# Kernel tuning notes

Hardware: AMD Instinct MI355X
Metric: run time of the kernel (lower is better)

## Reference

```python
import jax, jax.numpy as jnp
import numpy as np

B, N, QD = 2, 2048, 1024
HEADS, DIM_HEAD = 16, 64
INNER = HEADS * DIM_HEAD  # 1024
SCALE = DIM_HEAD ** -0.5


def setup_inputs() -> dict:
    key = jax.random.key(0)
    ks = jax.random.split(key, 8)
    x = jax.random.normal(ks[0], (B, N, QD), dtype=jnp.float32)
    bias = jax.random.normal(ks[1], (B, N, N), dtype=jnp.float32)
    mask = jax.random.randint(ks[2], (B, N), 0, 2) > 0
    # parameters (nn.Linear stores weight [out, in]; we keep [in, out] and matmul x @ W)
    Wq = jax.random.normal(ks[3], (QD, INNER), dtype=jnp.float32) * (QD ** -0.5)
    Wkv = jax.random.normal(ks[4], (QD, 2 * INNER), dtype=jnp.float32) * (QD ** -0.5)
    Wo = jax.random.normal(ks[5], (INNER, QD), dtype=jnp.float32) * (INNER ** -0.5)
    bo = jax.random.normal(ks[6], (QD,), dtype=jnp.float32) * 0.01
    return {"x": x, "bias": bias, "mask": mask, "Wq": Wq, "Wkv": Wkv, "Wo": Wo, "bo": bo}


def reference(x, bias, mask, Wq, Wkv, Wo, bo):
    b, n, _ = x.shape
    q = x @ Wq                      # [b, n, inner]
    kv = x @ Wkv                    # [b, n, 2*inner] (context defaults to x)
    k, v = jnp.split(kv, 2, axis=-1)
    # split heads: [b, h, n, d]
    split = lambda t: t.reshape(b, n, HEADS, DIM_HEAD).transpose(0, 2, 1, 3)
    q, k, v = split(q), split(k), split(v)
    sim = jnp.einsum('bhid,bhjd->bhij', q, k) * SCALE   # [b, h, n, n]
    sim = sim + bias[:, None, :, :]                      # additive bias broadcast over heads
    max_neg = -jnp.finfo(sim.dtype).max
    sim = jnp.where(mask[:, None, None, :], sim, max_neg)  # per-key mask
    attn = jax.nn.softmax(sim, axis=-1)
    out = jnp.einsum('bhij,bhjd->bhid', attn, v)         # [b, h, n, d]
    out = out.transpose(0, 2, 1, 3).reshape(b, n, INNER)  # merge heads
    return out @ Wo + bo
```

## Files before the change

kernel.cpp:

```cpp
#include <hip/hip_runtime.h>
#include <hip/hip_bf16.h>
#include <stdint.h>

#define B_     2
#define N_     2048
#define QD_    1024
#define H_     16
#define DH_    64
#define INNER_ 1024
#define SCALE_ 0.125f

typedef unsigned short u16;
typedef __attribute__((ext_vector_type(8))) short bf16x8;
typedef __attribute__((ext_vector_type(4))) float f32x4;
typedef __attribute__((ext_vector_type(4))) unsigned short u16x4;
typedef __attribute__((ext_vector_type(8))) unsigned short u16x8;

#define GLD16(gp, lp) __builtin_amdgcn_global_load_lds( \
    (const __attribute__((address_space(1))) unsigned int*)(gp), \
    (__attribute__((address_space(3))) unsigned int*)(lp), 16, 0, 0)

__device__ inline u16 f2bf(float f) {
    union { float f; uint32_t u; } c; c.f = f;
    uint32_t r = c.u + 0x7FFFu + ((c.u >> 16) & 1u);
    return (u16)(r >> 16);
}
__device__ inline float bf2f(u16 s) {
    union { uint32_t u; float f; } c; c.u = ((uint32_t)s) << 16;
    return c.f;
}
__device__ inline void split2(float v, u16 &h, u16 &l) {
    u16 hs = f2bf(v);
    h = hs;
    l = f2bf(v - bf2f(hs));
}
__device__ inline unsigned pk2(float a, float b) {
    float2 f; f.x = a; f.y = b;
    union { __hip_bfloat162 v; unsigned u; } c;
    c.v = __float22bfloat162_rn(f);
    return c.u;
}
__device__ inline float f4get(const float4& v, int r) {
    return r == 0 ? v.x : r == 1 ? v.y : r == 2 ? v.z : v.w;
}

__global__ __launch_bounds__(256) void prep_kernel(
    const float* __restrict__ x, u16* __restrict__ xh, u16* __restrict__ xl,
    const float* __restrict__ Wq, const float* __restrict__ Wkv, const float* __restrict__ Wo,
    u16* __restrict__ wTh, u16* __restrict__ wTl,
    u16* __restrict__ woTh, u16* __restrict__ woTl)
{
    __shared__ float t[32][33];
    const int blk = blockIdx.x, tid = threadIdx.x;
    if (blk < 4096) {
        int idx = blk * 256 + tid;
        float4 v = ((const float4*)x)[idx];
        u16x4 hv, lv; u16 h, l;
        split2(v.x, h, l); hv.x = h; lv.x = l;
        split2(v.y, h, l); hv.y = h; lv.y = l;
        split2(v.z, h, l); hv.z = h; lv.z = l;
        split2(v.w, h, l); hv.w = h; lv.w = l;
        ((u16x4*)xh)[idx] = hv;
        ((u16x4*)xl)[idx] = lv;
        return;
    }
    int local = blk - 4096;
    const float* src; u16 *dhi, *dlo; int C, bx, by;
    if (local < 1024)      { src = Wq;  dhi = wTh;                dlo = wTl;                C = 1024; by = local >> 5; bx = local & 31; }
    else if (local < 3072) { int l2 = local - 1024; src = Wkv; dhi = wTh + 1024 * 1024; dlo = wTl + 1024 * 1024; C = 2048; by = l2 >> 6; bx = l2 & 63; }
    else                   { int l2 = local - 3072; src = Wo;  dhi = woTh;               dlo = woTl;               C = 1024; by = l2 >> 5; bx = l2 & 31; }
    const int x0 = bx * 32, y0 = by * 32;
    const int tx = tid & 31, ty = tid >> 5;
    for (int yy = ty; yy < 32; yy += 8)
        t[yy][tx] = src[(size_t)(y0 + yy) * C + x0 + tx];
    __syncthreads();
    for (int i = ty; i < 32; i += 8) {
        float v = t[tx][i];
        u16 h, l; split2(v, h, l);
        size_t o = (size_t)(x0 + i) * 1024 + y0 + tx;
        dhi[o] = h; dlo[o] = l;
    }
}

__device__ inline void bias_read(int T, int bkoff, int bl16,
                                 const float* __restrict__ bias,
                                 const int* __restrict__ mask,
                                 float4 bR[4], int4& bM)
{
    int bb2 = T >> 10, rest = T & 1023;
    int k0b = (rest & 31) * 64, q0 = (rest >> 5) * 64;
    int kk = k0b + bkoff;
    bM = *(const int4*)&mask[bb2 * N_ + kk];
#pragma unroll
    for (int m = 0; m < 4; m++)
        bR[m] = *(const float4*)&bias[((size_t)bb2 * N_ + q0 + m * 16 + bl16) * N_ + kk];
}
__device__ inline void bias_store(int T, int bwvr, int blane, int bhf,
                                  const float4 bR[4], const int4& bM,
                                  u16* __restrict__ bsw)
{
    int bb2 = T >> 10, rest = T & 1023;
    int k0b = (rest & 31) * 64, q0 = (rest >> 5) * 64;
    int wv = ((k0b >> 5) & 3) + bwvr;
    const u16 NEG = f2bf(-1e30f);
    const int mok[4] = { bM.x, bM.y, bM.z, bM.w };
    u16x8 o0, o1;
#pragma unroll
    for (int i = 0; i < 8; i++) {
        int m = i >> 2, r = i & 3;
        o0[i] = mok[r] ? f2bf(f4get(bR[m], r)) : NEG;
    }
#pragma unroll
    for (int i = 0; i < 8; i++) {
        int m = 2 + (i >> 2), r = i & 3;
        o1[i] = mok[r] ? f2bf(f4get(bR[m], r)) : NEG;
    }
    size_t ob = ((((size_t)bb2 * 32 + (q0 >> 6)) * 16 + (k0b >> 7)) * 4 + wv) * 2048
                + (size_t)blane * 32 + bhf * 16;
    *(u16x8*)&bsw[ob]     = o0;
    *(u16x8*)&bsw[ob + 8] = o1;
}
__device__ inline void bias_block(int T, int tid,
                                  const float* __restrict__ bias,
                                  const int* __restrict__ mask,
                                  u16* __restrict__ bsw)
{
    const int bp = tid >> 1, bhf = tid & 1;
    const int blane = bp & 63, bquad = blane >> 4, bl16 = blane & 15;
    const int bwvr = bp >> 6;
    const int bkoff = bwvr * 32 + bquad * 8 + bhf * 4;
    float4 bR[4]; int4 bM;
    bias_read(T, bkoff, bl16, bias, mask, bR, bM);
    bias_store(T, bwvr, blane, bhf, bR, bM, bsw);
}

__global__ __launch_bounds__(256) void gemm_qkv_bias(
    int mode,
    const u16* __restrict__ Ah, const u16* __restrict__ Al,
    const u16* __restrict__ Bh,
    u16* __restrict__ qh,
    u16* __restrict__ kb, u16* __restrict__ vT,
    const float* __restrict__ bias, const int* __restrict__ mask,
    u16* __restrict__ bsw)
{
    __shared__ __align__(16) char smem[49152];
    const int tid = threadIdx.x;

    int gid = -1, bid = -1;
    if (mode == 1) {
        if (blockIdx.x < 768) gid = blockIdx.x; else bid = blockIdx.x - 768;
    } else if (mode == 0) gid = blockIdx.x;
    else bid = blockIdx.x;

    if (bid >= 0) {
        bias_block(bid, tid, bias, mask, bsw);
        return;
    }
    gid = (gid & 7) * 96 + (gid >> 3);

    const int wave = tid >> 6, lane = tid & 63;
    const int quad = lane >> 4, l16 = lane & 15;
    const int wm = wave >> 1, wn = wave & 1;
    const int bx = gid % 24, by = gid / 24;
    const int bm = by * 128, bn = bx * 128;
    const bool comp = (bx < 8);

    f32x4 acc[4][4];
#pragma unroll
    for (int i = 0; i < 4; i++)
#pragma unroll
        for (int j = 0; j < 4; j++) acc[i][j] = (f32x4){0.f, 0.f, 0.f, 0.f};

    const int row0 = tid >> 2, g4 = tid & 3;
    const int r1 = row0, r2 = row0 + 64;
    const int gc1 = (g4 ^ (r1 & 3)) * 8, gc2 = (g4 ^ (r2 & 3)) * 8;
    const size_t a1 = (size_t)(bm + r1) * 1024 + gc1, a2 = (size_t)(bm + r2) * 1024 + gc2;
    const size_t b1 = (size_t)(bn + r1) * 1024 + gc1, b2 = (size_t)(bn + r2) * 1024 + gc2;
    const int ldsw = wave * 1024;

    auto issue = [&](char* base, int kn) {
        GLD16(Ah + a1 + kn, base + ldsw);
        GLD16(Ah + a2 + kn, base + 4096 + ldsw);
        GLD16(Bh + b1 + kn, base + 16384 + ldsw);
        GLD16(Bh + b2 + kn, base + 20480 + ldsw);
        if (comp) {
            GLD16(Al + a1 + kn, base + 8192 + ldsw);
            GLD16(Al + a2 + kn, base + 12288 + ldsw);
        }
    };

    issue(smem, 0);
    int cur = 0;
    for (int k0 = 0; k0 < 1024; k0 += 32) {
        __syncthreads();
        char* cb_ = smem + cur * 24576;
        if (k0 + 32 < 1024) issue(smem + (cur ^ 1) * 24576, k0 + 32);
        const u16* cAh = (const u16*)cb_;
        const u16* cAl = (const u16*)(cb_ + 8192);
        const u16* cBh = (const u16*)(cb_ + 16384);
        bf16x8 fah[4], fal[4], fbh[4];
#pragma unroll
        for (int s = 0; s < 4; s++) {
            int ra = wm * 64 + s * 16 + l16;
            int rb = wn * 64 + s * 16 + l16;
            int ca = (quad ^ (ra & 3)) * 8;
            int cb = (quad ^ (rb & 3)) * 8;
            fah[s] = *(const bf16x8*)&cAh[ra * 32 + ca];
            fbh[s] = *(const bf16x8*)&cBh[rb * 32 + cb];
            if (comp) fal[s] = *(const bf16x8*)&cAl[ra * 32 + ca];
        }
#pragma unroll
        for (int sm = 0; sm < 4; sm++)
#pragma unroll
            for (int sn = 0; sn < 4; sn++) {
                acc[sm][sn] = __builtin_amdgcn_mfma_f32_16x16x32_bf16(fah[sm], fbh[sn], acc[sm][sn], 0, 0, 0);
                if (comp)
                    acc[sm][sn] = __builtin_amdgcn_mfma_f32_16x16x32_bf16(fal[sm], fbh[sn], acc[sm][sn], 0, 0, 0);
            }
        cur ^= 1;
    }
#pragma unroll
    for (int sm = 0; sm < 4; sm++) {
        int rowb = bm + wm * 64 + sm * 16 + quad * 4;
        int bb = rowb >> 11, i0 = rowb & 2047;
#pragma unroll
        for (int sn = 0; sn < 4; sn++) {
            int col = bn + wn * 64 + sn * 16 + l16;
            int region = col >> 10;
            int hh = (col >> 6) & 15;
            int d = col & 63;
            if (region == 0) {
#pragma unroll
                for (int r = 0; r < 4; r++) {
                    size_t o = (((size_t)(bb * H_ + hh)) * N_ + i0 + r) * DH_ + d;
                    qh[o] = f2bf(acc[sm][sn][r] * SCALE_);
                }
            } else if (region == 1) {
#pragma unroll
                for (int r = 0; r < 4; r++) {
                    size_t o = (((size_t)(bb * H_ + hh)) * N_ + i0 + r) * DH_ + d;
                    kb[o] = f2bf(acc[sm][sn][r]);
                }
            } else {
                u16x4 pv;
#pragma unroll
                for (int r = 0; r < 4; r++) pv[r] = f2bf(acc[sm][sn][r]);
                *(u16x4*)&vT[(((size_t)(bb * H_ + hh)) * DH_ + d) * N_ + i0] = pv;
            }
        }
    }
}

__global__ __launch_bounds__(256) void gemm_out(
    const u16* __restrict__ Ab,
    const u16* __restrict__ Bh,
    const float* __restrict__ bo, float* __restrict__ out)
{
    __shared__ __align__(16) char smem[24576];
    const int tid = threadIdx.x;
    const int wave = tid >> 6, lane = tid & 63;
    const int quad = lane >> 4, l16 = lane & 15;
    const int wm = wave >> 1, wn = wave & 1;
    const int bm = blockIdx.y * 128, bn = blockIdx.x * 64;

    f32x4 acc[4][2];
#pragma unroll
    for (int i = 0; i < 4; i++)
#pragma unroll
        for (int j = 0; j < 2; j++) acc[i][j] = (f32x4){0.f, 0.f, 0.f, 0.f};

    const int row0 = tid >> 2, g4 = tid & 3;
    const int r1 = row0, r2 = row0 + 64;
    const int gc1 = (g4 ^ (r1 & 3)) * 8, gc2 = (g4 ^ (r2 & 3)) * 8;
    const size_t a1 = (size_t)(bm + r1) * 1024 + gc1, a2 = (size_t)(bm + r2) * 1024 + gc2;
    const size_t bgo = (size_t)(bn + r1) * 1024 + gc1;
    const int ldsw = wave * 1024;

    auto issue = [&](char* base, int kn) {
        GLD16(Ab + a1 + kn, base + ldsw);
        GLD16(Ab + a2 + kn, base + 4096 + ldsw);
        GLD16(Bh + bgo + kn, base + 8192 + ldsw);
    };

    issue(smem, 0);
    int cur = 0;
    for (int k0 = 0; k0 < 1024; k0 += 32) {
        __syncthreads();
        char* cb_ = smem + cur * 12288;
        if (k0 + 32 < 1024) issue(smem + (cur ^ 1) * 12288, k0 + 32);
        const u16* cA  = (const u16*)cb_;
        const u16* cBh = (const u16*)(cb_ + 8192);
        bf16x8 fa[4], fbh[2];
#pragma unroll
        for (int s = 0; s < 4; s++) {
            int ra = wm * 64 + s * 16 + l16;
            int ca = (quad ^ (ra & 3)) * 8;
            fa[s] = *(const bf16x8*)&cA[ra * 32 + ca];
        }
#pragma unroll
        for (int s = 0; s < 2; s++) {
            int rb = wn * 32 + s * 16 + l16;
            int cb = (quad ^ (rb & 3)) * 8;
            fbh[s] = *(const bf16x8*)&cBh[rb * 32 + cb];
        }
#pragma unroll
        for (int sm = 0; sm < 4; sm++)
#pragma unroll
            for (int sn = 0; sn < 2; sn++)
                acc[sm][sn] = __builtin_amdgcn_mfma_f32_16x16x32_bf16(fa[sm], fbh[sn], acc[sm][sn], 0, 0, 0);
        cur ^= 1;
    }
#pragma unroll
    for (int sm = 0; sm < 4; sm++) {
        int rowb = bm + wm * 64 + sm * 16 + quad * 4;
#pragma unroll
        for (int sn = 0; sn < 2; sn++) {
            int col = bn + wn * 32 + sn * 16 + l16;
            float bv = bo[col];
#pragma unroll
            for (int r = 0; r < 4; r++)
                out[(size_t)(rowb + r) * 1024 + col] = acc[sm][sn][r] + bv;
        }
    }
}

#define LDK 72
#define LDV 128

__global__ __launch_bounds__(256, 2) void attn_kernel(
    const u16* __restrict__ qh,
    const u16* __restrict__ kb, const u16* __restrict__ vT,
    const u16* __restrict__ bsw, u16* __restrict__ ob)
{
    __shared__ __align__(16) char smem[35328];
    u16* sK  = (u16*)smem;
    u16* sVt = (u16*)(smem + 18432);
    float* rO = (float*)smem;
    float* rL = (float*)(smem + 34816);

    const int lin = blockIdx.x;
    const int xcd = lin & 7, slot = lin >> 3;
    const int bh = xcd * 4 + (slot >> 5);
    const int qt = slot & 31;
    const int b = bh >> 4, h = bh & 15;
    const int qbase = qt * 64;
    const int tid = threadIdx.x, wave = tid >> 6, lane = tid & 63;
    const int quad = lane >> 4, l16 = lane & 15;

    bf16x8 aq[4][2];
#pragma unroll
    for (int m = 0; m < 4; m++) {
        size_t qo = ((size_t)bh * N_ + qbase + m * 16 + l16) * DH_ + quad * 8;
        aq[m][0] = *(const bf16x8*)&qh[qo];
        aq[m][1] = *(const bf16x8*)&qh[qo + 32];
    }
    f32x4 Oacc[4][4], lacc[4];
#pragma unroll
    for (int m = 0; m < 4; m++) {
        lacc[m] = (f32x4){0.f, 0.f, 0.f, 0.f};
#pragma unroll
        for (int nd = 0; nd < 4; nd++) Oacc[m][nd] = (f32x4){0.f, 0.f, 0.f, 0.f};
    }
    bf16x8 ones;
#pragma unroll
    for (int i = 0; i < 8; i++) ones[i] = (short)0x3F80;

    const int rK = tid >> 3, cK = (tid & 7) * 8;
    const int sigK = ((rK & 4) << 2) + ((rK >> 3) << 2) + (rK & 3);
    const int rV = tid >> 4;
    const int vg = tid & 15;
    const int cV = vg * 8;
    const int vsw = (vg ^ (rV & 7)) * 8;
    const int vrg = ((wave * 4 + quad) ^ (l16 & 7)) * 8;
    const size_t kgbase = (size_t)bh * N_ * DH_;
    const size_t vgbase = (size_t)bh * DH_ * N_;
    const size_t bswb = (size_t)(b * 32 + qt) * 131072 + (size_t)wave * 2048
                        + (size_t)lane * 32;

    bf16x8 pK[4], pV[4];
    u16x8 cB[4], nB[4];
#pragma unroll
    for (int it = 0; it < 4; it++) {
        pK[it] = *(const bf16x8*)&kb[kgbase + (size_t)(rK + it * 32) * DH_ + cK];
        pV[it] = *(const bf16x8*)&vT[vgbase + (size_t)(rV + it * 16) * N_ + cV];
    }
#pragma unroll
    for (int c = 0; c < 4; c++) cB[c] = *(const u16x8*)&bsw[bswb + c * 8];

    for (int jt = 0; jt < 16; jt++) {
#pragma unroll
        for (int it = 0; it < 4; it++) {
            *(bf16x8*)&sK[(it * 32 + sigK) * LDK + cK] = pK[it];
            *(bf16x8*)&sVt[(rV + it * 16) * LDV + vsw] = pV[it];
        }
        __syncthreads();
        if (jt < 15) {
            int j0n = (jt + 1) * 128;
#pragma unroll
            for (int it = 0; it < 4; it++) {
                pK[it] = *(const bf16x8*)&kb[kgbase + (size_t)(j0n + rK + it * 32) * DH_ + cK];
                pV[it] = *(const bf16x8*)&vT[vgbase + (size_t)(rV + it * 16) * N_ + j0n + cV];
            }
            size_t bb = bswb + (size_t)(jt + 1) * 8192;
#pragma unroll
            for (int c = 0; c < 4; c++) nB[c] = *(const u16x8*)&bsw[bb + c * 8];
        }
        bf16x8 kf[2][2], vf[4];
#pragma unroll
        for (int n = 0; n < 2; n++)
#pragma unroll
            for (int s = 0; s < 2; s++)
                kf[n][s] = *(const bf16x8*)&sK[(wave * 32 + n * 16 + l16) * LDK + s * 32 + quad * 8];
#pragma unroll
        for (int nd = 0; nd < 4; nd++)
            vf[nd] = *(const bf16x8*)&sVt[(nd * 16 + l16) * LDV + vrg];

#pragma unroll
        for (int m = 0; m < 4; m++) {
            f32x4 S0 = (f32x4){0.f, 0.f, 0.f, 0.f};
            f32x4 S1 = (f32x4){0.f, 0.f, 0.f, 0.f};
#pragma unroll
            for (int s = 0; s < 2; s++) {
                S0 = __builtin_amdgcn_mfma_f32_16x16x32_bf16(kf[0][s], aq[m][s], S0, 0, 0, 0);
                S1 = __builtin_amdgcn_mfma_f32_16x16x32_bf16(kf[1][s], aq[m][s], S1, 0, 0, 0);
            }
            float p0[4], p1[4];
#pragma unroll
            for (int r = 0; r < 4; r++) {
                p0[r] = __expf(S0[r] + bf2f(cB[m >> 1][(m & 1) * 4 + r]));
                p1[r] = __expf(S1[r] + bf2f(cB[2 + (m >> 1)][(m & 1) * 4 + r]));
            }
            union { bf16x8 v; unsigned w[4]; } pa;
            pa.w[0] = pk2(p0[0], p0[1]);
            pa.w[1] = pk2(p0[2], p0[3]);
            pa.w[2] = pk2(p1[0], p1[1]);
            pa.w[3] = pk2(p1[2], p1[3]);
            lacc[m] = __builtin_amdgcn_mfma_f32_16x16x32_bf16(pa.v, ones, lacc[m], 0, 0, 0);
#pragma unroll
            for (int nd = 0; nd < 4; nd++)
                Oacc[m][nd] = __builtin_amdgcn_mfma_f32_16x16x32_bf16(pa.v, vf[nd], Oacc[m][nd], 0, 0, 0);
        }
#pragma unroll
        for (int c = 0; c < 4; c++) cB[c] = nB[c];
        __syncthreads();
    }

    if (wave >= 2) {
        int slot2 = wave - 2;
#pragma unroll
        for (int m = 0; m < 4; m++) {
#pragma unroll
            for (int nd = 0; nd < 4; nd++)
#pragma unroll
                for (int r = 0; r < 4; r++)
                    rO[(slot2 * 64 + m * 16 + quad * 4 + r) * 68 + nd * 16 + l16] = Oacc[m][nd][r];
            if (l16 == 0)
#pragma unroll
                for (int r = 0; r < 4; r++)
                    rL[slot2 * 64 + m * 16 + quad * 4 + r] = lacc[m][r];
        }
    }
    __syncthreads();
    if (wave < 2) {
        int slot2 = wave;
#pragma unroll
        for (int m = 0; m < 4; m++) {
#pragma unroll
            for (int nd = 0; nd < 4; nd++)
#pragma unroll
                for (int r = 0; r < 4; r++) {
                    int idx = (slot2 * 64 + m * 16 + quad * 4 + r) * 68 + nd * 16 + l16;
                    rO[idx] += Oacc[m][nd][r];
                }
            if (l16 == 0)
#pragma unroll
                for (int r = 0; r < 4; r++)
                    rL[slot2 * 64 + m * 16 + quad * 4 + r] += lacc[m][r];
        }
    }
    __syncthreads();
    {
        const int q = tid >> 2, dg = (tid & 3) * 16;
        float l = rL[q] + rL[64 + q];
        float inv = 1.f / l;
        f32x4 s[4];
#pragma unroll
        for (int i4 = 0; i4 < 4; i4++) {
            s[i4] = *(const f32x4*)&rO[(size_t)q * 68 + dg + i4 * 4];
            f32x4 v = *(const f32x4*)&rO[(size_t)(64 + q) * 68 + dg + i4 * 4];
            s[i4] += v;
        }
        size_t obase = ((size_t)b * N_ + qbase + q) * INNER_ + h * 64 + dg;
#pragma unroll
        for (int i4 = 0; i4 < 4; i4++) {
            u16x4 o4;
#pragma unroll
            for (int r = 0; r < 4; r++) o4[r] = f2bf(s[i4][r] * inv);
            *(u16x4*)&ob[obase + i4 * 4] = o4;
        }
    }
}

extern "C" void kernel_launch(void* const* d_in, const int* in_sizes, int n_in,
                              void* d_out, int out_size, void* d_ws, size_t ws_size,
                              hipStream_t stream)
{
    const float* x    = (const float*)d_in[0];
    const float* bias = (const float*)d_in[1];
    const int*   mask = (const int*)d_in[2];
    const float* Wq   = (const float*)d_in[3];
    const float* Wkv  = (const float*)d_in[4];
    const float* Wo   = (const float*)d_in[5];
    const float* bo   = (const float*)d_in[6];
    float* out = (float*)d_out;

    char* w = (char*)d_ws;
    const size_t MB = 1024 * 1024;
    u16* q_h   = (u16*)(w);
    u16* k_b   = (u16*)(w + 16 * MB);
    u16* v_T   = (u16*)(w + 24 * MB);
    u16* xs_h  = (u16*)(w + 32 * MB);
    u16* xs_l  = (u16*)(w + 40 * MB);
    u16* wT_h  = (u16*)(w + 48 * MB);
    u16* wT_l  = (u16*)(w + 54 * MB);
    u16* woT_h = (u16*)(w + 60 * MB);
    u16* woT_l = (u16*)(w + 62 * MB);
    u16* o_b   = (u16*)(w + 64 * MB);

    const size_t bsw_bytes = (size_t)2 * N_ * N_ * sizeof(u16);
    const bool concurrent = ws_size >= 72 * MB + bsw_bytes;

    prep_kernel<<<8192, 256, 0, stream>>>(x, xs_h, xs_l, Wq, Wkv, Wo, wT_h, wT_l, woT_h, woT_l);

    if (concurrent) {
        u16* bsw = (u16*)(w + 72 * MB);
        gemm_qkv_bias<<<2816, 256, 0, stream>>>(1, xs_h, xs_l, wT_h,
                                                q_h, k_b, v_T, bias, mask, bsw);
        attn_kernel<<<1024, 256, 0, stream>>>(q_h, k_b, v_T, bsw, o_b);
    } else {
        u16* bsw = (u16*)(w + 32 * MB);
        gemm_qkv_bias<<<768, 256, 0, stream>>>(0, xs_h, xs_l, wT_h,
                                               q_h, k_b, v_T, bias, mask, bsw);
        gemm_qkv_bias<<<2048, 256, 0, stream>>>(2, xs_h, xs_l, wT_h,
                                                q_h, k_b, v_T, bias, mask, bsw);
        attn_kernel<<<1024, 256, 0, stream>>>(q_h, k_b, v_T, bsw, o_b);
    }
    gemm_out<<<dim3(16, 32), 256, 0, stream>>>(o_b, woT_h, bo, out);
}
```

Measured before the change: 257.1 us.

## Split QKV GEMM into KV tiles and smaller Q tiles, drop XCD attention remap

Restructures the QKV projection into two block types. KV blocks use 128x128 tiles with a single bf16 pass, and Q blocks use 64x128 tiles with the hi/lo compensated pass, each with its own smaller LDS footprint. This lowers shared memory from 48KB to 32KB and balances per-block work, since the Q-region blocks previously did twice the MFMAs. The attention kernel also moves from an XCD-aware linear block remap to a plain 2D grid, which may change L2 locality of K/V across chiplets.

```diff
diff --git a/kernel.cpp b/kernel.cpp
--- a/kernel.cpp
+++ b/kernel.cpp
@@ -143,12 +143,12 @@
     const float* __restrict__ bias, const int* __restrict__ mask,
     u16* __restrict__ bsw)
 {
-    __shared__ __align__(16) char smem[49152];
+    __shared__ __align__(16) char smem[32768];
     const int tid = threadIdx.x;
 
     int gid = -1, bid = -1;
     if (mode == 1) {
-        if (blockIdx.x < 768) gid = blockIdx.x; else bid = blockIdx.x - 768;
+        if (blockIdx.x < 1024) gid = blockIdx.x; else bid = blockIdx.x - 1024;
     } else if (mode == 0) gid = blockIdx.x;
     else bid = blockIdx.x;
 
@@ -156,96 +156,143 @@
         bias_block(bid, tid, bias, mask, bsw);
         return;
     }
-    gid = (gid & 7) * 96 + (gid >> 3);
+    gid = (gid & 7) * 128 + (gid >> 3);
 
     const int wave = tid >> 6, lane = tid & 63;
     const int quad = lane >> 4, l16 = lane & 15;
     const int wm = wave >> 1, wn = wave & 1;
-    const int bx = gid % 24, by = gid / 24;
-    const int bm = by * 128, bn = bx * 128;
-    const bool comp = (bx < 8);
-
-    f32x4 acc[4][4];
-#pragma unroll
-    for (int i = 0; i < 4; i++)
-#pragma unroll
-        for (int j = 0; j < 4; j++) acc[i][j] = (f32x4){0.f, 0.f, 0.f, 0.f};
-
     const int row0 = tid >> 2, g4 = tid & 3;
-    const int r1 = row0, r2 = row0 + 64;
-    const int gc1 = (g4 ^ (r1 & 3)) * 8, gc2 = (g4 ^ (r2 & 3)) * 8;
-    const size_t a1 = (size_t)(bm + r1) * 1024 + gc1, a2 = (size_t)(bm + r2) * 1024 + gc2;
-    const size_t b1 = (size_t)(bn + r1) * 1024 + gc1, b2 = (size_t)(bn + r2) * 1024 + gc2;
+    const int gc1 = (g4 ^ (row0 & 3)) * 8, gc2 = (g4 ^ ((row0 + 64) & 3)) * 8;
     const int ldsw = wave * 1024;
 
-    auto issue = [&](char* base, int kn) {
-        GLD16(Ah + a1 + kn, base + ldsw);
-        GLD16(Ah + a2 + kn, base + 4096 + ldsw);
-        GLD16(Bh + b1 + kn, base + 16384 + ldsw);
-        GLD16(Bh + b2 + kn, base + 20480 + ldsw);
-        if (comp) {
-            GLD16(Al + a1 + kn, base + 8192 + ldsw);
-            GLD16(Al + a2 + kn, base + 12288 + ldsw);
-        }
-    };
-
-    issue(smem, 0);
-    int cur = 0;
-    for (int k0 = 0; k0 < 1024; k0 += 32) {
-        __syncthreads();
-        char* cb_ = smem + cur * 24576;
-        if (k0 + 32 < 1024) issue(smem + (cur ^ 1) * 24576, k0 + 32);
-        const u16* cAh = (const u16*)cb_;
-        const u16* cAl = (const u16*)(cb_ + 8192);
-        const u16* cBh = (const u16*)(cb_ + 16384);
-        bf16x8 fah[4], fal[4], fbh[4];
-#pragma unroll
-        for (int s = 0; s < 4; s++) {
-            int ra = wm * 64 + s * 16 + l16;
-            int rb = wn * 64 + s * 16 + l16;
-            int ca = (quad ^ (ra & 3)) * 8;
-            int cb = (quad ^ (rb & 3)) * 8;
-            fah[s] = *(const bf16x8*)&cAh[ra * 32 + ca];
-            fbh[s] = *(const bf16x8*)&cBh[rb * 32 + cb];
-            if (comp) fal[s] = *(const bf16x8*)&cAl[ra * 32 + ca];
-        }
-#pragma unroll
-        for (int sm = 0; sm < 4; sm++)
+    if (gid < 512) {
+        const int bm = (gid >> 4) * 128, bn = (8 + (gid & 15)) * 128;
+        f32x4 acc[4][4];
+#pragma unroll
+        for (int i = 0; i < 4; i++)
+#pragma unroll
+            for (int j = 0; j < 4; j++) acc[i][j] = (f32x4){0.f, 0.f, 0.f, 0.f};
+
+        const size_t a1 = (size_t)(bm + row0) * 1024 + gc1, a2 = (size_t)(bm + row0 + 64) * 1024 + gc2;
+        const size_t b1 = (size_t)(bn + row0) * 1024 + gc1, b2 = (size_t)(bn + row0 + 64) * 1024 + gc2;
+
+        auto issue = [&](char* base, int kn) {
+            GLD16(Ah + a1 + kn, base + ldsw);
+            GLD16(Ah + a2 + kn, base + 4096 + ldsw);
+            GLD16(Bh + b1 + kn, base + 8192 + ldsw);
+            GLD16(Bh + b2 + kn, base + 12288 + ldsw);
+        };
+
+        issue(smem, 0);
+        int cur = 0;
+        for (int k0 = 0; k0 < 1024; k0 += 32) {
+            __syncthreads();
+            char* cb_ = smem + cur * 16384;
+            if (k0 + 32 < 1024) issue(smem + (cur ^ 1) * 16384, k0 + 32);
+            const u16* cA = (const u16*)cb_;
+            const u16* cB = (const u16*)(cb_ + 8192);
+            bf16x8 fa[4], fb[4];
+#pragma unroll
+            for (int s = 0; s < 4; s++) {
+                int ra = wm * 64 + s * 16 + l16;
+                int rb = wn * 64 + s * 16 + l16;
+                fa[s] = *(const bf16x8*)&cA[ra * 32 + (quad ^ (ra & 3)) * 8];
+                fb[s] = *(const bf16x8*)&cB[rb * 32 + (quad ^ (rb & 3)) * 8];
+            }
+#pragma unroll
+            for (int sm = 0; sm < 4; sm++)
+#pragma unroll
+                for (int sn = 0; sn < 4; sn++)
+                    acc[sm][sn] = __builtin_amdgcn_mfma_f32_16x16x32_bf16(fa[sm], fb[sn], acc[sm][sn], 0, 0, 0);
+            cur ^= 1;
+        }
+#pragma unroll
+        for (int sm = 0; sm < 4; sm++) {
+            int rowb = bm + wm * 64 + sm * 16 + quad * 4;
+            int bb = rowb >> 11, i0 = rowb & 2047;
 #pragma unroll
             for (int sn = 0; sn < 4; sn++) {
-                acc[sm][sn] = __builtin_amdgcn_mfma_f32_16x16x32_bf16(fah[sm], fbh[sn], acc[sm][sn], 0, 0, 0);
-                if (comp)
-                    acc[sm][sn] = __builtin_amdgcn_mfma_f32_16x16x32_bf16(fal[sm], fbh[sn], acc[sm][sn], 0, 0, 0);
-            }
-        cur ^= 1;
-    }
-#pragma unroll
-    for (int sm = 0; sm < 4; sm++) {
-        int rowb = bm + wm * 64 + sm * 16 + quad * 4;
-        int bb = rowb >> 11, i0 = rowb & 2047;
-#pragma unroll
-        for (int sn = 0; sn < 4; sn++) {
-            int col = bn + wn * 64 + sn * 16 + l16;
-            int region = col >> 10;
-            int hh = (col >> 6) & 15;
-            int d = col & 63;
-            if (region == 0) {
+                int col = bn + wn * 64 + sn * 16 + l16;
+                int region = col >> 10;
+                int hh = (col >> 6) & 15;
+                int d = col & 63;
+                if (region == 1) {
+#pragma unroll
+                    for (int r = 0; r < 4; r++) {
+                        size_t o = (((size_t)(bb * H_ + hh)) * N_ + i0 + r) * DH_ + d;
+                        kb[o] = f2bf(acc[sm][sn][r]);
+                    }
+                } else {
+                    u16x4 pv;
+#pragma unroll
+                    for (int r = 0; r < 4; r++) pv[r] = f2bf(acc[sm][sn][r]);
+                    *(u16x4*)&vT[(((size_t)(bb * H_ + hh)) * DH_ + d) * N_ + i0] = pv;
+                }
+            }
+        }
+    } else {
+        const int g2 = gid - 512;
+        const int bm = (g2 >> 3) * 64, bn = (g2 & 7) * 128;
+        f32x4 acc[2][4];
+#pragma unroll
+        for (int i = 0; i < 2; i++)
+#pragma unroll
+            for (int j = 0; j < 4; j++) acc[i][j] = (f32x4){0.f, 0.f, 0.f, 0.f};
+
+        const size_t a1 = (size_t)(bm + row0) * 1024 + gc1;
+        const size_t b1 = (size_t)(bn + row0) * 1024 + gc1, b2 = (size_t)(bn + row0 + 64) * 1024 + gc2;
+
+        auto issue = [&](char* base, int kn) {
+            GLD16(Ah + a1 + kn, base + ldsw);
+            GLD16(Al + a1 + kn, base + 4096 + ldsw);
+            GLD16(Bh + b1 + kn, base + 8192 + ldsw);
+            GLD16(Bh + b2 + kn, base + 12288 + ldsw);
+        };
+
+        issue(smem, 0);
+        int cur = 0;
+        for (int k0 = 0; k0 < 1024; k0 += 32) {
+            __syncthreads();
+            char* cb_ = smem + cur * 16384;
+            if (k0 + 32 < 1024) issue(smem + (cur ^ 1) * 16384, k0 + 32);
+            const u16* cAh = (const u16*)cb_;
+            const u16* cAl = (const u16*)(cb_ + 4096);
+            const u16* cB  = (const u16*)(cb_ + 8192);
+            bf16x8 fah[2], fal[2], fb[4];
+#pragma unroll
+            for (int s = 0; s < 2; s++) {
+                int ra = wm * 32 + s * 16 + l16;
+                int ca = (quad ^ (ra & 3)) * 8;
+                fah[s] = *(const bf16x8*)&cAh[ra * 32 + ca];
+                fal[s] = *(const bf16x8*)&cAl[ra * 32 + ca];
+            }
+#pragma unroll
+            for (int s = 0; s < 4; s++) {
+                int rb = wn * 64 + s * 16 + l16;
+                fb[s] = *(const bf16x8*)&cB[rb * 32 + (quad ^ (rb & 3)) * 8];
+            }
+#pragma unroll
+            for (int sm = 0; sm < 2; sm++)
+#pragma unroll
+                for (int sn = 0; sn < 4; sn++) {
+                    acc[sm][sn] = __builtin_amdgcn_mfma_f32_16x16x32_bf16(fah[sm], fb[sn], acc[sm][sn], 0, 0, 0);
+                    acc[sm][sn] = __builtin_amdgcn_mfma_f32_16x16x32_bf16(fal[sm], fb[sn], acc[sm][sn], 0, 0, 0);
+                }
+            cur ^= 1;
+        }
+#pragma unroll
+        for (int sm = 0; sm < 2; sm++) {
+            int rowb = bm + wm * 32 + sm * 16 + quad * 4;
+            int bb = rowb >> 11, i0 = rowb & 2047;
+#pragma unroll
+            for (int sn = 0; sn < 4; sn++) {
+                int col = bn + wn * 64 + sn * 16 + l16;
+                int hh = col >> 6, d = col & 63;
 #pragma unroll
                 for (int r = 0; r < 4; r++) {
                     size_t o = (((size_t)(bb * H_ + hh)) * N_ + i0 + r) * DH_ + d;
                     qh[o] = f2bf(acc[sm][sn][r] * SCALE_);
                 }
-            } else if (region == 1) {
-#pragma unroll
-                for (int r = 0; r < 4; r++) {
-                    size_t o = (((size_t)(bb * H_ + hh)) * N_ + i0 + r) * DH_ + d;
-                    kb[o] = f2bf(acc[sm][sn][r]);
-                }
-            } else {
-                u16x4 pv;
-#pragma unroll
-                for (int r = 0; r < 4; r++) pv[r] = f2bf(acc[sm][sn][r]);
-                *(u16x4*)&vT[(((size_t)(bb * H_ + hh)) * DH_ + d) * N_ + i0] = pv;
             }
         }
     }
@@ -338,12 +385,8 @@
     float* rO = (float*)smem;
     float* rL = (float*)(smem + 34816);
 
-    const int lin = blockIdx.x;
-    const int xcd = lin & 7, slot = lin >> 3;
-    const int bh = xcd * 4 + (slot >> 5);
-    const int qt = slot & 31;
-    const int b = bh >> 4, h = bh & 15;
-    const int qbase = qt * 64;
+    const int bh = blockIdx.y, b = bh >> 4, h = bh & 15;
+    const int qt = blockIdx.x, qbase = qt * 64;
     const int tid = threadIdx.x, wave = tid >> 6, lane = tid & 63;
     const int quad = lane >> 4, l16 = lane & 15;
 
@@ -446,36 +489,36 @@
     }
 
     if (wave >= 2) {
-        int slot2 = wave - 2;
+        int slot = wave - 2;
 #pragma unroll
         for (int m = 0; m < 4; m++) {
 #pragma unroll
             for (int nd = 0; nd < 4; nd++)
 #pragma unroll
                 for (int r = 0; r < 4; r++)
-                    rO[(slot2 * 64 + m * 16 + quad * 4 + r) * 68 + nd * 16 + l16] = Oacc[m][nd][r];
+                    rO[(slot * 64 + m * 16 + quad * 4 + r) * 68 + nd * 16 + l16] = Oacc[m][nd][r];
             if (l16 == 0)
 #pragma unroll
                 for (int r = 0; r < 4; r++)
-                    rL[slot2 * 64 + m * 16 + quad * 4 + r] = lacc[m][r];
+                    rL[slot * 64 + m * 16 + quad * 4 + r] = lacc[m][r];
         }
     }
     __syncthreads();
     if (wave < 2) {
-        int slot2 = wave;
+        int slot = wave;
 #pragma unroll
         for (int m = 0; m < 4; m++) {
 #pragma unroll
             for (int nd = 0; nd < 4; nd++)
 #pragma unroll
                 for (int r = 0; r < 4; r++) {
-                    int idx = (slot2 * 64 + m * 16 + quad * 4 + r) * 68 + nd * 16 + l16;
+                    int idx = (slot * 64 + m * 16 + quad * 4 + r) * 68 + nd * 16 + l16;
                     rO[idx] += Oacc[m][nd][r];
                 }
             if (l16 == 0)
 #pragma unroll
                 for (int r = 0; r < 4; r++)
-                    rL[slot2 * 64 + m * 16 + quad * 4 + r] += lacc[m][r];
+                    rL[slot * 64 + m * 16 + quad * 4 + r] += lacc[m][r];
         }
     }
     __syncthreads();
@@ -534,16 +577,16 @@
 
     if (concurrent) {
         u16* bsw = (u16*)(w + 72 * MB);
-        gemm_qkv_bias<<<2816, 256, 0, stream>>>(1, xs_h, xs_l, wT_h,
+        gemm_qkv_bias<<<3072, 256, 0, stream>>>(1, xs_h, xs_l, wT_h,
                                                 q_h, k_b, v_T, bias, mask, bsw);
-        attn_kernel<<<1024, 256, 0, stream>>>(q_h, k_b, v_T, bsw, o_b);
+        attn_kernel<<<dim3(32, 32), 256, 0, stream>>>(q_h, k_b, v_T, bsw, o_b);
     } else {
         u16* bsw = (u16*)(w + 32 * MB);
-        gemm_qkv_bias<<<768, 256, 0, stream>>>(0, xs_h, xs_l, wT_h,
-                                               q_h, k_b, v_T, bias, mask, bsw);
+        gemm_qkv_bias<<<1024, 256, 0, stream>>>(0, xs_h, xs_l, wT_h,
+                                                q_h, k_b, v_T, bias, mask, bsw);
         gemm_qkv_bias<<<2048, 256, 0, stream>>>(2, xs_h, xs_l, wT_h,
                                                 q_h, k_b, v_T, bias, mask, bsw);
-        attn_kernel<<<1024, 256, 0, stream>>>(q_h, k_b, v_T, bsw, o_b);
+        attn_kernel<<<dim3(32, 32), 256, 0, stream>>>(q_h, k_b, v_T, bsw, o_b);
     }
     gemm_out<<<dim3(16, 32), 256, 0, stream>>>(o_b, woT_h, bo, out);
 }
```

Measured after the change: 239.8 us. 1.07x faster.
